# Optimization experiments

Measured on AMD Instinct MI355X. Metric: run time of the kernel, lower is better.

Reference implementation:

```python
import jax, jax.numpy as jnp
import numpy as np

N_NODES = 100000
PAIRNORM_EPS = 1e-5


def add_self_loops(edge_index, n):
    loops = jnp.arange(n, dtype=edge_index.dtype)
    src = jnp.concatenate([edge_index[0], loops])
    dst = jnp.concatenate([edge_index[1], loops])
    return src, dst


def gcn_norm(src, dst, n):
    # symmetric normalization D^-1/2 (A+I) D^-1/2, degree over targets (PyG flow source_to_target)
    deg = jax.ops.segment_sum(jnp.ones(dst.shape, jnp.float32), dst, num_segments=n)
    dinv = jnp.where(deg > 0, jax.lax.rsqrt(deg), 0.0)
    return dinv[src] * dinv[dst]  # [E]


def gcn_conv(x, src, dst, norm, W, b, n):
    h = x @ W                                   # [N, out]
    msg = h[src] * norm[:, None]                # gather + scale
    out = jax.ops.segment_sum(msg, dst, num_segments=n)  # scatter-add
    return out + b


def pairnorm(x):
    xc = x - jnp.mean(x, axis=0, keepdims=True)
    scale = jax.lax.rsqrt(PAIRNORM_EPS + jnp.mean(jnp.sum(xc * xc, axis=-1)))
    return xc * scale


def setup_inputs() -> dict:
    key = jax.random.key(0)
    ks = jax.random.split(key, 8)
    n, e, d_in, d_h, n_cls = N_NODES, 3200000, 512, 32, 40
    return {
        "x": jax.random.normal(ks[0], (n, d_in), jnp.float32),
        "edge_index": jax.random.randint(ks[1], (2, e), 0, n, jnp.int64),
        "W0": jax.random.normal(ks[2], (d_in, d_h), jnp.float32) * (1.0 / np.sqrt(d_in)),
        "b0": jnp.zeros((d_h,), jnp.float32),
        "W1": jax.random.normal(ks[3], (d_h, d_h), jnp.float32) * (1.0 / np.sqrt(d_h)),
        "b1": jnp.zeros((d_h,), jnp.float32),
        "Wf": jax.random.normal(ks[4], (d_h, n_cls), jnp.float32) * (1.0 / np.sqrt(d_h)),
        "bf": jnp.zeros((n_cls,), jnp.float32),
    }


def reference(x, edge_index, W0, b0, W1, b1, Wf, bf):
    n = x.shape[0]
    # drop_edge keep_ratio = 1.0 -> all edges kept each layer
    src, dst = add_self_loops(edge_index, n)
    norm = gcn_norm(src, dst, n)
    h = gcn_conv(x, src, dst, norm, W0, b0, n)
    h = jax.nn.relu(pairnorm(h))
    h = gcn_conv(h, src, dst, norm, W1, b1, n)
    h = jax.nn.relu(pairnorm(h))
    out = gcn_conv(h, src, dst, norm, Wf, bf, n)
    return out
```

## Files before the change

kernel.cpp:

```cpp
#include <hip/hip_runtime.h>
#include <hip/hip_bf16.h>

typedef __attribute__((ext_vector_type(8))) short bf16x8;
typedef __attribute__((ext_vector_type(4))) float f32x4;

#define NPB 512
#define EPB 8192

static __device__ __forceinline__ short f2bf(float v) {
  union { float f; unsigned u; } c; c.f = v;
  unsigned r = c.u + 0x7fffu + ((c.u >> 16) & 1u);
  return (short)(r >> 16);
}

__global__ void zero_int(int* p, int n) {
  int i = blockIdx.x * blockDim.x + threadIdx.x;
  if (i < n) p[i] = 0;
}
__global__ void make_dinv2(const int* __restrict__ cnt, float* __restrict__ dinv, int n) {
  int i = blockIdx.x * blockDim.x + threadIdx.x;
  if (i < n) dinv[i] = rsqrtf(1.0f + (float)cnt[i]);
}

__global__ __launch_bounds__(256) void bucket_hist(const int* __restrict__ dst,
                                                   int* __restrict__ bucket_cnt, int e, int nb) {
  __shared__ int lh[256];
  int t = threadIdx.x;
  lh[t] = 0;
  __syncthreads();
  int c0 = blockIdx.x * EPB, c1 = min(c0 + EPB, e);
  for (int i = c0 + t; i < c1; i += 256) atomicAdd(&lh[dst[i] >> 9], 1);
  __syncthreads();
  if (t < nb && lh[t] > 0) atomicAdd(&bucket_cnt[t], lh[t]);
}
__global__ void bucket_scan(const int* __restrict__ bucket_cnt, int* __restrict__ base,
                            int* __restrict__ gcursor, int nb, int e) {
  __shared__ int s[256];
  int t = threadIdx.x;
  int v = (t < nb) ? bucket_cnt[t] : 0;
  s[t] = v;
  __syncthreads();
  for (int off = 1; off < 256; off <<= 1) {
    int val = (t >= off) ? s[t - off] : 0;
    __syncthreads();
    s[t] += val;
    __syncthreads();
  }
  if (t < nb) { int b = s[t] - v; base[t] = b; gcursor[t] = b; }
  if (t == 0) base[nb] = e;
}
__global__ __launch_bounds__(256) void bucket_partition(const int* __restrict__ src,
    const int* __restrict__ dst, int* __restrict__ gcursor, int* __restrict__ ebuf,
    int e, int nb) {
  __shared__ int lh[256];
  __shared__ int lbase[256];
  int t = threadIdx.x;
  lh[t] = 0;
  __syncthreads();
  int c0 = blockIdx.x * EPB, c1 = min(c0 + EPB, e);
  for (int i = c0 + t; i < c1; i += 256) atomicAdd(&lh[dst[i] >> 9], 1);
  __syncthreads();
  if (t < nb && lh[t] > 0) lbase[t] = atomicAdd(&gcursor[t], lh[t]);
  lh[t] = 0;
  __syncthreads();
  for (int i = c0 + t; i < c1; i += 256) {
    int d = dst[i], b = d >> 9;
    int r = atomicAdd(&lh[b], 1);
    ebuf[lbase[b] + r] = ((d & (NPB - 1)) << 17) | src[i];
  }
}
__global__ __launch_bounds__(256) void node_count(const int* __restrict__ ebuf,
    const int* __restrict__ base, int* __restrict__ cnt, int n) {
  __shared__ int lc[NPB];
  int b = blockIdx.x;
  for (int i = threadIdx.x; i < NPB; i += 256) lc[i] = 0;
  __syncthreads();
  int b0 = base[b], b1 = base[b + 1];
  for (int i = b0 + threadIdx.x; i < b1; i += 256) atomicAdd(&lc[ebuf[i] >> 17], 1);
  __syncthreads();
  int g0 = b * NPB;
  for (int i = threadIdx.x; i < NPB; i += 256)
    if (g0 + i < n) cnt[g0 + i] = lc[i];
}
__global__ __launch_bounds__(256) void scan1(const int* __restrict__ cnt, int* __restrict__ excl,
                                             int* __restrict__ blksum, int n) {
  __shared__ int tsum[256];
  int t = threadIdx.x;
  int idx = blockIdx.x * 1024 + t * 4;
  int4 v = {0, 0, 0, 0};
  if (idx + 3 < n) v = *(const int4*)(cnt + idx);
  else {
    if (idx < n) v.x = cnt[idx];
    if (idx + 1 < n) v.y = cnt[idx + 1];
    if (idx + 2 < n) v.z = cnt[idx + 2];
    if (idx + 3 < n) v.w = cnt[idx + 3];
  }
  int s = v.x + v.y + v.z + v.w;
  tsum[t] = s;
  __syncthreads();
  for (int off = 1; off < 256; off <<= 1) {
    int val = (t >= off) ? tsum[t - off] : 0;
    __syncthreads();
    tsum[t] += val;
    __syncthreads();
  }
  int e0 = tsum[t] - s;
  if (idx < n) excl[idx] = e0;
  if (idx + 1 < n) excl[idx + 1] = e0 + v.x;
  if (idx + 2 < n) excl[idx + 2] = e0 + v.x + v.y;
  if (idx + 3 < n) excl[idx + 3] = e0 + v.x + v.y + v.z;
  if (t == 255) blksum[blockIdx.x] = tsum[255];
}
__global__ void scan2(const int* __restrict__ blksum, int* __restrict__ blkoff, int nb) {
  __shared__ int s[256];
  int t = threadIdx.x;
  int v0 = (t < nb) ? blksum[t] : 0;
  s[t] = v0;
  __syncthreads();
  for (int off = 1; off < 256; off <<= 1) {
    int val = (t >= off) ? s[t - off] : 0;
    __syncthreads();
    s[t] += val;
    __syncthreads();
  }
  if (t < nb) blkoff[t] = s[t] - v0;
}
__global__ void scan3(int* __restrict__ rowptr, const int* __restrict__ blkoff, int n, int e) {
  int i = blockIdx.x * blockDim.x + threadIdx.x;
  if (i < n) rowptr[i] += blkoff[i >> 10];
  if (i == 0) rowptr[n] = e;
}
__global__ __launch_bounds__(256) void bucket_scatter(const int* __restrict__ ebuf,
    const int* __restrict__ base, const int* __restrict__ rowptr,
    int* __restrict__ ssrc, int n) {
  __shared__ int lcur[NPB];
  int b = blockIdx.x;
  int g0 = b * NPB;
  for (int i = threadIdx.x; i < NPB; i += 256)
    lcur[i] = (g0 + i < n) ? rowptr[g0 + i] : 0;
  __syncthreads();
  int b0 = base[b], b1 = base[b + 1];
  for (int i = b0 + threadIdx.x; i < b1; i += 256) {
    int p = ebuf[i];
    int pos = atomicAdd(&lcur[p >> 17], 1);
    ssrc[pos] = p & 0x1FFFF;
  }
}

__global__ __launch_bounds__(256) void gemm0_mfma(
    const float* __restrict__ x, const float* __restrict__ W,
    const float* __restrict__ dinv, float* __restrict__ h, int n) {
  __shared__ bf16x8 wp[2048];
  int tid = threadIdx.x;
  for (int s = tid; s < 2048; s += 256) {
    int ct = s >> 10, rem = s & 1023, ks = rem >> 6, lane = rem & 63;
    int r = lane & 15, half = lane >> 4;
    int k0 = ks * 32 + half * 8;
    bf16x8 tmp;
#pragma unroll
    for (int j = 0; j < 8; ++j)
      tmp[j] = f2bf(W[(k0 + j) * 32 + ct * 16 + r]);
    wp[s] = tmp;
  }
  __syncthreads();
  int wave = tid >> 6, lane = tid & 63;
  int rowbase = blockIdx.x * 64 + wave * 16;
  int r = lane & 15, half = lane >> 4;
  int arow = rowbase + r; if (arow > n - 1) arow = n - 1;
  const float* xr = x + (size_t)arow * 512 + half * 8;
  f32x4 acc0 = {0.f, 0.f, 0.f, 0.f}, acc1 = {0.f, 0.f, 0.f, 0.f};
#pragma unroll
  for (int ks = 0; ks < 16; ++ks) {
    f32x4 a0 = *(const f32x4*)(xr + ks * 32);
    f32x4 a1 = *(const f32x4*)(xr + ks * 32 + 4);
    bf16x8 af;
    af[0] = f2bf(a0[0]); af[1] = f2bf(a0[1]); af[2] = f2bf(a0[2]); af[3] = f2bf(a0[3]);
    af[4] = f2bf(a1[0]); af[5] = f2bf(a1[1]); af[6] = f2bf(a1[2]); af[7] = f2bf(a1[3]);
    acc0 = __builtin_amdgcn_mfma_f32_16x16x32_bf16(af, wp[ks * 64 + lane], acc0, 0, 0, 0);
    acc1 = __builtin_amdgcn_mfma_f32_16x16x32_bf16(af, wp[1024 + ks * 64 + lane], acc1, 0, 0, 0);
  }
#pragma unroll
  for (int rg = 0; rg < 4; ++rg) {
    int row = rowbase + half * 4 + rg;
    if (row < n) {
      float dv = dinv[row];
      h[(size_t)row * 32 + r]      = acc0[rg] * dv;
      h[(size_t)row * 32 + 16 + r] = acc1[rg] * dv;
    }
  }
}

__global__ __launch_bounds__(256) void agg_gather32(
    const float* __restrict__ h, const float* __restrict__ dinv,
    const float* __restrict__ bias, const int* __restrict__ rowptr,
    const int* __restrict__ ssrc, float* __restrict__ out, int n) {
  int wid = (int)((blockIdx.x * 256u + threadIdx.x) >> 6);
  int lane = threadIdx.x & 63;
  if (wid >= n) return;
  int f = lane & 31;
  int r0 = rowptr[wid], r1 = rowptr[wid + 1];
  float self = h[(size_t)wid * 32 + f];
  float acc = 0.f;
  int j = r0 + (lane >> 5);
  for (; j + 6 < r1; j += 8) {
    int s0 = ssrc[j], s1 = ssrc[j + 2], s2 = ssrc[j + 4], s3 = ssrc[j + 6];
    float v0 = h[(size_t)s0 * 32 + f], v1 = h[(size_t)s1 * 32 + f];
    float v2 = h[(size_t)s2 * 32 + f], v3 = h[(size_t)s3 * 32 + f];
    acc += v0 + v1 + v2 + v3;
  }
  for (; j < r1; j += 2) acc += h[(size_t)ssrc[j] * 32 + f];
  acc += __shfl_down(acc, 32, 64);
  if (lane < 32)
    out[(size_t)wid * 32 + f] = bias[f] + dinv[wid] * (self + acc);
}
__global__ __launch_bounds__(256) void agg_gather40(
    const float* __restrict__ h, const float* __restrict__ dinv,
    const float* __restrict__ bias, const int* __restrict__ rowptr,
    const int* __restrict__ ssrc, float* __restrict__ out, int n) {
  int wid = (int)((blockIdx.x * 256u + threadIdx.x) >> 6);
  int lane = threadIdx.x & 63;
  if (wid >= n) return;
  int r0 = rowptr[wid], r1 = rowptr[wid + 1];
  float self = (lane < 40) ? h[(size_t)wid * 40 + lane] : 0.f;
  float acc = 0.f;
  int j = r0;
  for (; j + 3 < r1; j += 4) {
    int s0 = ssrc[j], s1 = ssrc[j + 1], s2 = ssrc[j + 2], s3 = ssrc[j + 3];
    if (lane < 40) {
      acc += h[(size_t)s0 * 40 + lane] + h[(size_t)s1 * 40 + lane]
           + h[(size_t)s2 * 40 + lane] + h[(size_t)s3 * 40 + lane];
    }
  }
  for (; j < r1; ++j)
    if (lane < 40) acc += h[(size_t)ssrc[j] * 40 + lane];
  if (lane < 40)
    out[(size_t)wid * 40 + lane] = bias[lane] + dinv[wid] * (self + acc);
}

__global__ void count_dst(const int* __restrict__ dst, int* __restrict__ cnt, int e) {
  int i = blockIdx.x * blockDim.x + threadIdx.x;
  if (i < e) atomicAdd(&cnt[dst[i]], 1);
}
template <int F>
__global__ void agg_init(const float* __restrict__ h, const float* __restrict__ dinv,
                         const float* __restrict__ bias, float* __restrict__ out, int n) {
  int idx = blockIdx.x * blockDim.x + threadIdx.x;
  if (idx >= n * F) return;
  int i = idx / F, f = idx - i * F;
  out[idx] = bias[f] + h[idx] * dinv[i];
}
template <int F>
__global__ void agg_edges(const float* __restrict__ h, const float* __restrict__ dinv,
                          const int* __restrict__ src, const int* __restrict__ dst,
                          float* __restrict__ out, int e) {
  int t = blockIdx.x * blockDim.x + threadIdx.x;
  int edge = t / F, f = t - edge * F;
  if (edge >= e) return;
  int s = src[edge], d = dst[edge];
  atomicAdd(&out[d * F + f], h[s * F + f] * dinv[d]);
}

__global__ void zero_stats(float* stats) {
  if (threadIdx.x < 40) stats[threadIdx.x] = 0.f;
}
__global__ void pn_stats(const float* __restrict__ x, float* __restrict__ stats, int n) {
  int tid = threadIdx.x;
  int gsize = gridDim.x * blockDim.x;
  float csum = 0.f, ssq = 0.f;
  for (int idx = blockIdx.x * blockDim.x + tid; idx < n * 32; idx += gsize) {
    float v = x[idx];
    csum += v; ssq += v * v;
  }
#pragma unroll
  for (int off = 32; off >= 1; off >>= 1) ssq += __shfl_down(ssq, off, 64);
  csum += __shfl_down(csum, 32, 64);
  __shared__ float scs[4 * 32];
  __shared__ float sss[4];
  int w = tid >> 6, lane = tid & 63;
  if (lane < 32) scs[w * 32 + lane] = csum;
  if (lane == 0) sss[w] = ssq;
  __syncthreads();
  if (tid < 32) atomicAdd(&stats[tid], scs[tid] + scs[32 + tid] + scs[64 + tid] + scs[96 + tid]);
  if (tid == 0) atomicAdd(&stats[32], sss[0] + sss[1] + sss[2] + sss[3]);
}
__global__ void pn_finalize(float* stats, float inv_n) {
  int f = threadIdx.x;
  float ssq = stats[32];
  float mu = (f < 32) ? stats[f] * inv_n : 0.f;
  float m2 = mu * mu;
#pragma unroll
  for (int off = 32; off >= 1; off >>= 1) m2 += __shfl_down(m2, off, 64);
  if (f < 32) stats[f] = mu;
  if (f == 0) stats[32] = rsqrtf(1e-5f + ssq * inv_n - m2);
}
__global__ void pn_apply(float* __restrict__ x, const float* __restrict__ stats, int n) {
  int idx = blockIdx.x * blockDim.x + threadIdx.x;
  if (idx >= n * 32) return;
  int f = idx & 31;
  float v = (x[idx] - stats[f]) * stats[32];
  x[idx] = v > 0.f ? v : 0.f;
}

template <int FIN, int FOUT>
__global__ void gemm_small(const float* __restrict__ x, const float* __restrict__ W,
                           const float* __restrict__ dinv, float* __restrict__ out, int n) {
  __shared__ float Ws[FIN * FOUT];
  for (int i = threadIdx.x; i < FIN * FOUT; i += blockDim.x) Ws[i] = W[i];
  __syncthreads();
  int t = blockIdx.x * blockDim.x + threadIdx.x;
  int i = t / FOUT, c = t - i * FOUT;
  if (i >= n) return;
  const float* xr = x + (size_t)i * FIN;
  float acc = 0.f;
#pragma unroll
  for (int k = 0; k < FIN; ++k) acc += xr[k] * Ws[k * FOUT + c];
  out[(size_t)i * FOUT + c] = acc * dinv[i];
}

static inline int cdiv(long long a, long long b) { return (int)((a + b - 1) / b); }

extern "C" void kernel_launch(void* const* d_in, const int* in_sizes, int n_in,
                              void* d_out, int out_size, void* d_ws, size_t ws_size,
                              hipStream_t stream) {
  const float* x   = (const float*)d_in[0];
  const int*   ei  = (const int*)d_in[1];
  const float* W0  = (const float*)d_in[2];
  const float* b0  = (const float*)d_in[3];
  const float* W1  = (const float*)d_in[4];
  const float* b1  = (const float*)d_in[5];
  const float* Wf  = (const float*)d_in[6];
  const float* bfi = (const float*)d_in[7];
  float* out = (float*)d_out;

  int n = in_sizes[0] / 512;
  int e = in_sizes[1] / 2;
  const int* src = ei;
  const int* dst = ei + e;

  char* ws = (char*)d_ws;
  size_t o = 0;
  auto alloc = [&](size_t bytes) { char* p = ws + o; o = (o + bytes + 255) & ~(size_t)255; return p; };
  int*   cnt   = (int*)alloc((size_t)n * 4);
  float* dinv  = (float*)alloc((size_t)n * 4);
  float* stats = (float*)alloc(256);
  float* bufA  = (float*)alloc((size_t)n * 40 * 4);
  size_t fallback_need = o;
  int*   rowptr = (int*)alloc((size_t)(n + 1) * 4);
  int*   blksum = (int*)alloc(1024);
  int*   blkoff = (int*)alloc(1024);
  int*   bucket_cnt  = (int*)alloc(256 * 4);
  int*   bucket_base = (int*)alloc(257 * 4);
  int*   gcursor     = (int*)alloc(256 * 4);
  int*   ssrc   = (int*)alloc((size_t)e * 4);
  size_t csr_need = o;

  int* ebuf = (int*)bufA;
  float* bufB = out;

  int NBk = cdiv(n, NPB);
  int nb2 = cdiv(n, 1024);
  bool use_csr = (ws_size >= csr_need) && (n <= 131072) && (NBk <= 256) && (nb2 <= 256) &&
                 ((size_t)n * 40 * 4 >= (size_t)e * 4);

  if (use_csr) {
    zero_int<<<1, 256, 0, stream>>>(bucket_cnt, NBk);
    bucket_hist<<<cdiv(e, EPB), 256, 0, stream>>>(dst, bucket_cnt, e, NBk);
    bucket_scan<<<1, 256, 0, stream>>>(bucket_cnt, bucket_base, gcursor, NBk, e);
    bucket_partition<<<cdiv(e, EPB), 256, 0, stream>>>(src, dst, gcursor, ebuf, e, NBk);
    node_count<<<NBk, 256, 0, stream>>>(ebuf, bucket_base, cnt, n);
    make_dinv2<<<cdiv(n, 256), 256, 0, stream>>>(cnt, dinv, n);
    scan1<<<nb2, 256, 0, stream>>>(cnt, rowptr, blksum, n);
    scan2<<<1, 256, 0, stream>>>(blksum, blkoff, nb2);
    scan3<<<cdiv(n, 256), 256, 0, stream>>>(rowptr, blkoff, n, e);
    bucket_scatter<<<NBk, 256, 0, stream>>>(ebuf, bucket_base, rowptr, ssrc, n);
  } else {
    zero_int<<<cdiv(n, 256), 256, 0, stream>>>(cnt, n);
    count_dst<<<cdiv(e, 256), 256, 0, stream>>>(dst, cnt, e);
    make_dinv2<<<cdiv(n, 256), 256, 0, stream>>>(cnt, dinv, n);
  }

  gemm0_mfma<<<cdiv(n, 64), 256, 0, stream>>>(x, W0, dinv, bufA, n);
  if (use_csr) {
    agg_gather32<<<cdiv(n, 4), 256, 0, stream>>>(bufA, dinv, b0, rowptr, ssrc, bufB, n);
  } else {
    agg_init<32><<<cdiv((long long)n * 32, 256), 256, 0, stream>>>(bufA, dinv, b0, bufB, n);
    agg_edges<32><<<cdiv((long long)e * 32, 256), 256, 0, stream>>>(bufA, dinv, src, dst, bufB, e);
  }
  zero_stats<<<1, 64, 0, stream>>>(stats);
  pn_stats<<<400, 256, 0, stream>>>(bufB, stats, n);
  pn_finalize<<<1, 64, 0, stream>>>(stats, 1.0f / n);
  pn_apply<<<cdiv((long long)n * 32, 256), 256, 0, stream>>>(bufB, stats, n);

  gemm_small<32, 32><<<cdiv((long long)n * 32, 256), 256, 0, stream>>>(bufB, W1, dinv, bufA, n);
  if (use_csr) {
    agg_gather32<<<cdiv(n, 4), 256, 0, stream>>>(bufA, dinv, b1, rowptr, ssrc, bufB, n);
  } else {
    agg_init<32><<<cdiv((long long)n * 32, 256), 256, 0, stream>>>(bufA, dinv, b1, bufB, n);
    agg_edges<32><<<cdiv((long long)e * 32, 256), 256, 0, stream>>>(bufA, dinv, src, dst, bufB, e);
  }
  zero_stats<<<1, 64, 0, stream>>>(stats);
  pn_stats<<<400, 256, 0, stream>>>(bufB, stats, n);
  pn_finalize<<<1, 64, 0, stream>>>(stats, 1.0f / n);
  pn_apply<<<cdiv((long long)n * 32, 256), 256, 0, stream>>>(bufB, stats, n);

  gemm_small<32, 40><<<cdiv((long long)n * 40, 320), 320, 0, stream>>>(bufB, Wf, dinv, bufA, n);
  if (use_csr) {
    agg_gather40<<<cdiv(n, 4), 256, 0, stream>>>(bufA, dinv, bfi, rowptr, ssrc, out, n);
  } else {
    agg_init<40><<<cdiv((long long)n * 40, 256), 256, 0, stream>>>(bufA, dinv, bfi, out, n);
    agg_edges<40><<<cdiv((long long)e * 40, 256), 256, 0, stream>>>(bufA, dinv, src, dst, out, e);
  }
}
```

Before: 804.3 us.

## Store transformed features in bf16 and fuse PairNorm apply into small GEMMs

The intermediate per-layer feature matrices h that feed the gather aggregations are now stored as bf16 instead of fp32, which halves the bytes fetched by the random neighbour gathers. The PairNorm apply plus ReLU step is folded into the following small GEMM, removing one read-modify-write pass over the node features per layer. The dinv computation is folded into node_count, dropping a separate launch. The cost is reduced precision in the aggregated messages, and 16-bit gathers in which each lane loads only 2 bytes.

```diff
diff --git a/kernel.cpp b/kernel.cpp
--- a/kernel.cpp
+++ b/kernel.cpp
@@ -8,9 +8,11 @@
 #define EPB 8192
 
 static __device__ __forceinline__ short f2bf(float v) {
-  union { float f; unsigned u; } c; c.f = v;
-  unsigned r = c.u + 0x7fffu + ((c.u >> 16) & 1u);
-  return (short)(r >> 16);
+  __hip_bfloat16 b = __float2bfloat16(v);
+  return __builtin_bit_cast(short, b);
+}
+static __device__ __forceinline__ float bf2f(unsigned short u) {
+  union { unsigned u; float f; } c; c.u = (unsigned)u << 16; return c.f;
 }
 
 __global__ void zero_int(int* p, int n) {
@@ -70,7 +72,7 @@
   }
 }
 __global__ __launch_bounds__(256) void node_count(const int* __restrict__ ebuf,
-    const int* __restrict__ base, int* __restrict__ cnt, int n) {
+    const int* __restrict__ base, int* __restrict__ cnt, float* __restrict__ dinv, int n) {
   __shared__ int lc[NPB];
   int b = blockIdx.x;
   for (int i = threadIdx.x; i < NPB; i += 256) lc[i] = 0;
@@ -80,7 +82,11 @@
   __syncthreads();
   int g0 = b * NPB;
   for (int i = threadIdx.x; i < NPB; i += 256)
-    if (g0 + i < n) cnt[g0 + i] = lc[i];
+    if (g0 + i < n) {
+      int c = lc[i];
+      cnt[g0 + i] = c;
+      dinv[g0 + i] = rsqrtf(1.0f + (float)c);
+    }
 }
 __global__ __launch_bounds__(256) void scan1(const int* __restrict__ cnt, int* __restrict__ excl,
                                              int* __restrict__ blksum, int n) {
@@ -149,7 +155,7 @@
 
 __global__ __launch_bounds__(256) void gemm0_mfma(
     const float* __restrict__ x, const float* __restrict__ W,
-    const float* __restrict__ dinv, float* __restrict__ h, int n) {
+    const float* __restrict__ dinv, unsigned short* __restrict__ hb, int n) {
   __shared__ bf16x8 wp[2048];
   int tid = threadIdx.x;
   for (int s = tid; s < 2048; s += 256) {
@@ -184,14 +190,14 @@
     int row = rowbase + half * 4 + rg;
     if (row < n) {
       float dv = dinv[row];
-      h[(size_t)row * 32 + r]      = acc0[rg] * dv;
-      h[(size_t)row * 32 + 16 + r] = acc1[rg] * dv;
+      hb[(size_t)row * 32 + r]      = (unsigned short)f2bf(acc0[rg] * dv);
+      hb[(size_t)row * 32 + 16 + r] = (unsigned short)f2bf(acc1[rg] * dv);
     }
   }
 }
 
 __global__ __launch_bounds__(256) void agg_gather32(
-    const float* __restrict__ h, const float* __restrict__ dinv,
+    const unsigned short* __restrict__ hb, const float* __restrict__ dinv,
     const float* __restrict__ bias, const int* __restrict__ rowptr,
     const int* __restrict__ ssrc, float* __restrict__ out, int n) {
   int wid = (int)((blockIdx.x * 256u + threadIdx.x) >> 6);
@@ -199,40 +205,40 @@
   if (wid >= n) return;
   int f = lane & 31;
   int r0 = rowptr[wid], r1 = rowptr[wid + 1];
-  float self = h[(size_t)wid * 32 + f];
+  float self = bf2f(hb[(size_t)wid * 32 + f]);
   float acc = 0.f;
   int j = r0 + (lane >> 5);
   for (; j + 6 < r1; j += 8) {
     int s0 = ssrc[j], s1 = ssrc[j + 2], s2 = ssrc[j + 4], s3 = ssrc[j + 6];
-    float v0 = h[(size_t)s0 * 32 + f], v1 = h[(size_t)s1 * 32 + f];
-    float v2 = h[(size_t)s2 * 32 + f], v3 = h[(size_t)s3 * 32 + f];
+    float v0 = bf2f(hb[(size_t)s0 * 32 + f]), v1 = bf2f(hb[(size_t)s1 * 32 + f]);
+    float v2 = bf2f(hb[(size_t)s2 * 32 + f]), v3 = bf2f(hb[(size_t)s3 * 32 + f]);
     acc += v0 + v1 + v2 + v3;
   }
-  for (; j < r1; j += 2) acc += h[(size_t)ssrc[j] * 32 + f];
+  for (; j < r1; j += 2) acc += bf2f(hb[(size_t)ssrc[j] * 32 + f]);
   acc += __shfl_down(acc, 32, 64);
   if (lane < 32)
     out[(size_t)wid * 32 + f] = bias[f] + dinv[wid] * (self + acc);
 }
 __global__ __launch_bounds__(256) void agg_gather40(
-    const float* __restrict__ h, const float* __restrict__ dinv,
+    const unsigned short* __restrict__ hb, const float* __restrict__ dinv,
     const float* __restrict__ bias, const int* __restrict__ rowptr,
     const int* __restrict__ ssrc, float* __restrict__ out, int n) {
   int wid = (int)((blockIdx.x * 256u + threadIdx.x) >> 6);
   int lane = threadIdx.x & 63;
   if (wid >= n) return;
   int r0 = rowptr[wid], r1 = rowptr[wid + 1];
-  float self = (lane < 40) ? h[(size_t)wid * 40 + lane] : 0.f;
+  float self = (lane < 40) ? bf2f(hb[(size_t)wid * 40 + lane]) : 0.f;
   float acc = 0.f;
   int j = r0;
   for (; j + 3 < r1; j += 4) {
     int s0 = ssrc[j], s1 = ssrc[j + 1], s2 = ssrc[j + 2], s3 = ssrc[j + 3];
     if (lane < 40) {
-      acc += h[(size_t)s0 * 40 + lane] + h[(size_t)s1 * 40 + lane]
-           + h[(size_t)s2 * 40 + lane] + h[(size_t)s3 * 40 + lane];
+      acc += bf2f(hb[(size_t)s0 * 40 + lane]) + bf2f(hb[(size_t)s1 * 40 + lane])
+           + bf2f(hb[(size_t)s2 * 40 + lane]) + bf2f(hb[(size_t)s3 * 40 + lane]);
     }
   }
   for (; j < r1; ++j)
-    if (lane < 40) acc += h[(size_t)ssrc[j] * 40 + lane];
+    if (lane < 40) acc += bf2f(hb[(size_t)ssrc[j] * 40 + lane]);
   if (lane < 40)
     out[(size_t)wid * 40 + lane] = bias[lane] + dinv[wid] * (self + acc);
 }
@@ -242,22 +248,22 @@
   if (i < e) atomicAdd(&cnt[dst[i]], 1);
 }
 template <int F>
-__global__ void agg_init(const float* __restrict__ h, const float* __restrict__ dinv,
+__global__ void agg_init(const unsigned short* __restrict__ hb, const float* __restrict__ dinv,
                          const float* __restrict__ bias, float* __restrict__ out, int n) {
   int idx = blockIdx.x * blockDim.x + threadIdx.x;
   if (idx >= n * F) return;
   int i = idx / F, f = idx - i * F;
-  out[idx] = bias[f] + h[idx] * dinv[i];
+  out[idx] = bias[f] + bf2f(hb[idx]) * dinv[i];
 }
 template <int F>
-__global__ void agg_edges(const float* __restrict__ h, const float* __restrict__ dinv,
+__global__ void agg_edges(const unsigned short* __restrict__ hb, const float* __restrict__ dinv,
                           const int* __restrict__ src, const int* __restrict__ dst,
                           float* __restrict__ out, int e) {
   int t = blockIdx.x * blockDim.x + threadIdx.x;
   int edge = t / F, f = t - edge * F;
   if (edge >= e) return;
   int s = src[edge], d = dst[edge];
-  atomicAdd(&out[d * F + f], h[s * F + f] * dinv[d]);
+  atomicAdd(&out[d * F + f], bf2f(hb[s * F + f]) * dinv[d]);
 }
 
 __global__ void zero_stats(float* stats) {
@@ -293,28 +299,32 @@
   if (f < 32) stats[f] = mu;
   if (f == 0) stats[32] = rsqrtf(1e-5f + ssq * inv_n - m2);
 }
-__global__ void pn_apply(float* __restrict__ x, const float* __restrict__ stats, int n) {
-  int idx = blockIdx.x * blockDim.x + threadIdx.x;
-  if (idx >= n * 32) return;
-  int f = idx & 31;
-  float v = (x[idx] - stats[f]) * stats[32];
-  x[idx] = v > 0.f ? v : 0.f;
-}
-
-template <int FIN, int FOUT>
-__global__ void gemm_small(const float* __restrict__ x, const float* __restrict__ W,
-                           const float* __restrict__ dinv, float* __restrict__ out, int n) {
-  __shared__ float Ws[FIN * FOUT];
-  for (int i = threadIdx.x; i < FIN * FOUT; i += blockDim.x) Ws[i] = W[i];
-  __syncthreads();
-  int t = blockIdx.x * blockDim.x + threadIdx.x;
-  int i = t / FOUT, c = t - i * FOUT;
+
+template <int FOUT>
+__global__ void gemm_small_pn(const float* __restrict__ x, const float* __restrict__ W,
+                              const float* __restrict__ stats, const float* __restrict__ dinv,
+                              unsigned short* __restrict__ outb, int n) {
+  __shared__ float Ws[32 * FOUT];
+  __shared__ float mu[32];
+  __shared__ float ssc[1];
+  int t = threadIdx.x;
+  for (int i = t; i < 32 * FOUT; i += blockDim.x) Ws[i] = W[i];
+  if (t < 32) mu[t] = stats[t];
+  if (t == 32) ssc[0] = stats[32];
+  __syncthreads();
+  float s = ssc[0];
+  int idx = blockIdx.x * blockDim.x + t;
+  int i = idx / FOUT, c = idx - i * FOUT;
   if (i >= n) return;
-  const float* xr = x + (size_t)i * FIN;
+  const float* xr = x + (size_t)i * 32;
   float acc = 0.f;
 #pragma unroll
-  for (int k = 0; k < FIN; ++k) acc += xr[k] * Ws[k * FOUT + c];
-  out[(size_t)i * FOUT + c] = acc * dinv[i];
+  for (int k = 0; k < 32; ++k) {
+    float v = (xr[k] - mu[k]) * s;
+    v = v > 0.f ? v : 0.f;
+    acc += v * Ws[k * FOUT + c];
+  }
+  outb[(size_t)i * FOUT + c] = (unsigned short)f2bf(acc * dinv[i]);
 }
 
 static inline int cdiv(long long a, long long b) { return (int)((a + b - 1) / b); }
@@ -343,7 +353,7 @@
   int*   cnt   = (int*)alloc((size_t)n * 4);
   float* dinv  = (float*)alloc((size_t)n * 4);
   float* stats = (float*)alloc(256);
-  float* bufA  = (float*)alloc((size_t)n * 40 * 4);
+  char*  hbuf  = alloc((size_t)n * 40 * 4);
   size_t fallback_need = o;
   int*   rowptr = (int*)alloc((size_t)(n + 1) * 4);
   int*   blksum = (int*)alloc(1024);
@@ -354,7 +364,9 @@
   int*   ssrc   = (int*)alloc((size_t)e * 4);
   size_t csr_need = o;
 
-  int* ebuf = (int*)bufA;
+  int* ebuf = (int*)hbuf;
+  unsigned short* hb   = (unsigned short*)hbuf;
+  unsigned short* hb40 = (unsigned short*)hbuf;
   float* bufB = out;
 
   int NBk = cdiv(n, NPB);
@@ -367,8 +379,7 @@
     bucket_hist<<<cdiv(e, EPB), 256, 0, stream>>>(dst, bucket_cnt, e, NBk);
     bucket_scan<<<1, 256, 0, stream>>>(bucket_cnt, bucket_base, gcursor, NBk, e);
     bucket_partition<<<cdiv(e, EPB), 256, 0, stream>>>(src, dst, gcursor, ebuf, e, NBk);
-    node_count<<<NBk, 256, 0, stream>>>(ebuf, bucket_base, cnt, n);
-    make_dinv2<<<cdiv(n, 256), 256, 0, stream>>>(cnt, dinv, n);
+    node_count<<<NBk, 256, 0, stream>>>(ebuf, bucket_base, cnt, dinv, n);
     scan1<<<nb2, 256, 0, stream>>>(cnt, rowptr, blksum, n);
     scan2<<<1, 256, 0, stream>>>(blksum, blkoff, nb2);
     scan3<<<cdiv(n, 256), 256, 0, stream>>>(rowptr, blkoff, n, e);
@@ -379,35 +390,33 @@
     make_dinv2<<<cdiv(n, 256), 256, 0, stream>>>(cnt, dinv, n);
   }
 
-  gemm0_mfma<<<cdiv(n, 64), 256, 0, stream>>>(x, W0, dinv, bufA, n);
+  gemm0_mfma<<<cdiv(n, 64), 256, 0, stream>>>(x, W0, dinv, hb, n);
   if (use_csr) {
-    agg_gather32<<<cdiv(n, 4), 256, 0, stream>>>(bufA, dinv, b0, rowptr, ssrc, bufB, n);
+    agg_gather32<<<cdiv(n, 4), 256, 0, stream>>>(hb, dinv, b0, rowptr, ssrc, bufB, n);
   } else {
-    agg_init<32><<<cdiv((long long)n * 32, 256), 256, 0, stream>>>(bufA, dinv, b0, bufB, n);
-    agg_edges<32><<<cdiv((long long)e * 32, 256), 256, 0, stream>>>(bufA, dinv, src, dst, bufB, e);
+    agg_init<32><<<cdiv((long long)n * 32, 256), 256, 0, stream>>>(hb, dinv, b0, bufB, n);
+    agg_edges<32><<<cdiv((long long)e * 32, 256), 256, 0, stream>>>(hb, dinv, src, dst, bufB, e);
   }
   zero_stats<<<1, 64, 0, stream>>>(stats);
   pn_stats<<<400, 256, 0, stream>>>(bufB, stats, n);
   pn_finalize<<<1, 64, 0, stream>>>(stats, 1.0f / n);
-  pn_apply<<<cdiv((long long)n * 32, 256), 256, 0, stream>>>(bufB, stats, n);
-
-  gemm_small<32, 32><<<cdiv((long long)n * 32, 256), 256, 0, stream>>>(bufB, W1, dinv, bufA, n);
+
+  gemm_small_pn<32><<<cdiv((long long)n * 32, 256), 256, 0, stream>>>(bufB, W1, stats, dinv, hb, n);
   if (use_csr) {
-    agg_gather32<<<cdiv(n, 4), 256, 0, stream>>>(bufA, dinv, b1, rowptr, ssrc, bufB, n);
+    agg_gather32<<<cdiv(n, 4), 256, 0, stream>>>(hb, dinv, b1, rowptr, ssrc, bufB, n);
   } else {
-    agg_init<32><<<cdiv((long long)n * 32, 256), 256, 0, stream>>>(bufA, dinv, b1, bufB, n);
-    agg_edges<32><<<cdiv((long long)e * 32, 256), 256, 0, stream>>>(bufA, dinv, src, dst, bufB, e);
+    agg_init<32><<<cdiv((long long)n * 32, 256), 256, 0, stream>>>(hb, dinv, b1, bufB, n);
+    agg_edges<32><<<cdiv((long long)e * 32, 256), 256, 0, stream>>>(hb, dinv, src, dst, bufB, e);
   }
   zero_stats<<<1, 64, 0, stream>>>(stats);
   pn_stats<<<400, 256, 0, stream>>>(bufB, stats, n);
   pn_finalize<<<1, 64, 0, stream>>>(stats, 1.0f / n);
-  pn_apply<<<cdiv((long long)n * 32, 256), 256, 0, stream>>>(bufB, stats, n);
-
-  gemm_small<32, 40><<<cdiv((long long)n * 40, 320), 320, 0, stream>>>(bufB, Wf, dinv, bufA, n);
+
+  gemm_small_pn<40><<<cdiv((long long)n * 40, 320), 320, 0, stream>>>(bufB, Wf, stats, dinv, hb40, n);
   if (use_csr) {
-    agg_gather40<<<cdiv(n, 4), 256, 0, stream>>>(bufA, dinv, bfi, rowptr, ssrc, out, n);
+    agg_gather40<<<cdiv(n, 4), 256, 0, stream>>>(hb40, dinv, bfi, rowptr, ssrc, out, n);
   } else {
-    agg_init<40><<<cdiv((long long)n * 40, 256), 256, 0, stream>>>(bufA, dinv, bfi, out, n);
-    agg_edges<40><<<cdiv((long long)e * 40, 256), 256, 0, stream>>>(bufA, dinv, src, dst, out, e);
-  }
-}
+    agg_init<40><<<cdiv((long long)n * 40, 256), 256, 0, stream>>>(hb40, dinv, bfi, out, n);
+    agg_edges<40><<<cdiv((long long)e * 40, 256), 256, 0, stream>>>(hb40, dinv, src, dst, out, e);
+  }
+}
```

New measurement: 779.6 us. 3.1% less time.
